# Kernel optimization log

Hardware: AMD Instinct MI355X
Metric: run time of the kernel (lower is better)

Reference implementation:

```python
import jax, jax.numpy as jnp
import numpy as np

DIM_U = 36
IDX_E = np.arange(0, 36, 2)   # even nodes (u1)
IDX_O = np.arange(1, 36, 2)   # odd nodes (u2)
# wraparound neighbor index sets (precomputed mod 36, matching torch negative indexing)
IDX_A = np.arange(-1, 34, 2) % 36   # [35,1,3,...,33]
IDX_B = np.arange(1, 36, 2)         # [1,3,...,35]
IDX_C = np.arange(3, 38, 2) % 36    # [3,5,...,35,1]


def setup_inputs() -> dict:
    key = jax.random.key(0)
    ks = jax.random.split(key, 9)
    N, H = 500000, 128
    return {
        "t": 0,
        "u": jax.random.normal(ks[0], (N, DIM_U), dtype=jnp.float32),
        "reg1": jax.random.normal(ks[1], (6,), dtype=jnp.float32),
        "reg2": jax.random.normal(ks[2], (4,), dtype=jnp.float32),
        "W1": jax.random.normal(ks[3], (18, H), dtype=jnp.float32) * 0.1,
        "b1": jax.random.normal(ks[4], (H,), dtype=jnp.float32) * 0.1,
        "W2a": jax.random.normal(ks[5], (H, 18 * 3), dtype=jnp.float32) * 0.1,
        "b2a": jax.random.normal(ks[6], (18 * 3,), dtype=jnp.float32) * 0.1,
        "W2b": jax.random.normal(ks[7], (H, 18 * 4), dtype=jnp.float32) * 0.1,
        "b2b": jax.random.normal(ks[8], (18 * 4,), dtype=jnp.float32) * 0.1,
    }


def _forward(u, reg1, reg2, W1, b1, W2a, b2a, W2b, b2b):
    N = u.shape[0]
    ie = IDX_E
    # features for even nodes: [N, 18, 5]
    x1 = jnp.stack([
        u[:, ie],
        u[:, (ie + 1) % DIM_U],
        u[:, (ie - 2) % DIM_U] * u[:, (ie - 1) % DIM_U],
        u[:, (ie - 1) % DIM_U] * u[:, (ie + 2) % DIM_U],
        u[:, ie] * u[:, (ie + 1) % DIM_U],
    ], axis=-1)
    io = IDX_O
    # features for odd nodes: [N, 18, 3]
    x2 = jnp.stack([
        u[:, io],
        u[:, (io - 2) % DIM_U] * u[:, (io - 1) % DIM_U],
        u[:, (io - 1) % DIM_U] * u[:, (io + 1) % DIM_U],
    ], axis=-1)
    outreg = jnp.zeros_like(u)
    outreg = outreg.at[:, IDX_E].set(jnp.einsum('nij,j->ni', x1, reg1[1:]) + reg1[0])
    outreg = outreg.at[:, IDX_O].set(jnp.einsum('nij,j->ni', x2, reg2[1:]) + reg2[0])
    # --- neural (cgnn) part: MLP 18 -> H -> (18*3, 18*4) ---
    u1 = u[:, IDX_E]                      # [N, 18]
    h = jnp.tanh(u1 @ W1 + b1)            # [N, H]
    out0 = (h @ W2a + b2a).reshape(N, 18, 3)
    out1 = (h @ W2b + b2b).reshape(N, 18, 4)
    uA, uB, uC = u[:, IDX_A], u[:, IDX_B], u[:, IDX_C]
    outnet = jnp.zeros_like(u)
    outnet = outnet.at[:, IDX_E].set(out0[:, :, 0] + out0[:, :, 1] * uA + out0[:, :, 2] * uB)
    outnet = outnet.at[:, IDX_O].set(out1[:, :, 0] + out1[:, :, 1] * uA + out1[:, :, 2] * uB + out1[:, :, 3] * uC)
    return outnet + outreg


def reference(t, u, reg1, reg2, W1, b1, W2a, b2a, W2b, b2b):
    return _forward(u, reg1, reg2, W1, b1, W2a, b2a, W2b, b2b)
```

## Files before the change

kernel.cpp:

```cpp
#include <hip/hip_runtime.h>
#include <cstddef>


typedef __attribute__((ext_vector_type(8))) __bf16 bf16x8;
typedef __attribute__((ext_vector_type(8))) short short8;
typedef __attribute__((ext_vector_type(4))) float f32x4;

__device__ __forceinline__ unsigned short f2bf(float f) {
    unsigned int u = __float_as_uint(f);
    unsigned int r = (u + 0x7FFFu + ((u >> 16) & 1u)) >> 16;
    return (unsigned short)r;
}

template <typename A>
__device__ __forceinline__ auto mfma_try(A a, A b, f32x4 c, int)
    -> decltype(__builtin_amdgcn_mfma_f32_16x16x32_bf16(a, b, c, 0, 0, 0)) {
    return __builtin_amdgcn_mfma_f32_16x16x32_bf16(a, b, c, 0, 0, 0);
}
template <typename A>
__device__ __forceinline__ f32x4 mfma_try(A a, A b, f32x4 c, long) {
    return __builtin_amdgcn_mfma_f32_16x16x32_bf16(
        __builtin_bit_cast(short8, a), __builtin_bit_cast(short8, b), c, 0, 0, 0);
}
__device__ __forceinline__ f32x4 mfma_bf16(short8 a, short8 b, f32x4 c) {
    return mfma_try(__builtin_bit_cast(bf16x8, a), __builtin_bit_cast(bf16x8, b), c, 0);
}

__device__ __forceinline__ float tanh_fast(float x) {
    const float e2 = __expf(2.0f * x);
    return 1.0f - __fdividef(2.0f, e2 + 1.0f);
}

__global__ __launch_bounds__(256, 4) void mixmodel_mfma6(
    const float* __restrict__ u,
    const float* __restrict__ reg1,
    const float* __restrict__ reg2,
    const float* __restrict__ W1,
    const float* __restrict__ b1,
    const float* __restrict__ W2a,
    const float* __restrict__ b2a,
    const float* __restrict__ W2b,
    const float* __restrict__ b2b,
    float* __restrict__ out,
    int N, int ntiles)
{
    __shared__ __align__(16) float          u_sh[2][32 * 38];
    __shared__ __align__(16) unsigned short h_sh[32 * 136];
    __shared__ __align__(16) float          c2s[32 * 132];

    const int tid = threadIdx.x;
    const int wid = tid >> 6;
    const int l   = tid & 63;
    const int ln  = l & 15;
    const int lg  = l >> 4;
    const int nb  = wid * 32;

    short8 b1f[2];
    short8 b2f[2][4];
    float bias1[2], bias2[2];
#pragma unroll
    for (int t = 0; t < 2; ++t) {
        const int n = nb + t * 16 + ln;
        short8 v;
#pragma unroll
        for (int j = 0; j < 8; ++j) {
            const int k = lg * 8 + j;
            const float w = (k < 18) ? W1[k * 128 + n] : 0.0f;
            v[j] = (short)f2bf(w);
        }
        b1f[t] = v;
        bias1[t] = b1[n];
        bias2[t] = (n < 54) ? b2a[n] : (n < 126 ? b2b[n - 54] : 0.0f);
#pragma unroll
        for (int kk = 0; kk < 4; ++kk) {
            short8 w2;
#pragma unroll
            for (int j = 0; j < 8; ++j) {
                const int k = kk * 32 + lg * 8 + j;
                float w;
                if (n < 54)       w = W2a[k * 54 + n];
                else if (n < 126) w = W2b[k * 72 + (n - 54)];
                else              w = 0.0f;
                w2[j] = (short)f2bf(w);
            }
            b2f[t][kk] = w2;
        }
    }

    const float r10 = reg1[0], r11 = reg1[1], r12 = reg1[2];
    const float r13 = reg1[3], r14 = reg1[4], r15 = reg1[5];
    const float r20 = reg2[0], r21 = reg2[1], r22 = reg2[2], r23 = reg2[3];

    const float4* ug = reinterpret_cast<const float4*>(u);
    const long fmax4 = (long)N * 9 - 1;
    const int gs = gridDim.x;

    const int idx0 = tid;
    const int row0 = idx0 / 9, c0 = idx0 - row0 * 9;
    const int idx1 = 256 + tid;
    const int row1 = idx1 / 9, c1 = idx1 - row1 * 9;

    float4 pf0, pf1;
    {
        long g0 = (long)blockIdx.x * 288 + idx0; if (g0 > fmax4) g0 = fmax4;
        pf0 = ug[g0];
        if (tid < 32) {
            long g1 = (long)blockIdx.x * 288 + idx1; if (g1 > fmax4) g1 = fmax4;
            pf1 = ug[g1];
        }
    }

    int b = 0;
    for (int tile = blockIdx.x; tile < ntiles; tile += gs) {
        {
            float* dst = &u_sh[b][row0 * 38 + c0 * 4];
            reinterpret_cast<float2*>(dst)[0] = make_float2(pf0.x, pf0.y);
            reinterpret_cast<float2*>(dst)[1] = make_float2(pf0.z, pf0.w);
            if (tid < 32) {
                float* dst1 = &u_sh[b][row1 * 38 + c1 * 4];
                reinterpret_cast<float2*>(dst1)[0] = make_float2(pf1.x, pf1.y);
                reinterpret_cast<float2*>(dst1)[1] = make_float2(pf1.z, pf1.w);
            }
            if (tile + gs < ntiles) {
                long g0 = (long)(tile + gs) * 288 + idx0; if (g0 > fmax4) g0 = fmax4;
                pf0 = ug[g0];
                if (tid < 32) {
                    long g1 = (long)(tile + gs) * 288 + idx1; if (g1 > fmax4) g1 = fmax4;
                    pf1 = ug[g1];
                }
            }
        }
        __syncthreads();

#pragma unroll
        for (int rb = 0; rb < 2; ++rb) {
            const float* urow = &u_sh[b][(rb * 16 + ln) * 38];
            short8 a1;
#pragma unroll
            for (int j = 0; j < 8; ++j) {
                const int k = lg * 8 + j;
                const float v = (k < 18) ? urow[2 * k] : 0.0f;
                a1[j] = (short)f2bf(v);
            }
#pragma unroll
            for (int t = 0; t < 2; ++t) {
                f32x4 c = bias1[t];
                const f32x4 h4 = mfma_bf16(a1, b1f[t], c);
#pragma unroll
                for (int r = 0; r < 4; ++r)
                    h_sh[(rb * 16 + lg * 4 + r) * 136 + nb + t * 16 + ln] =
                        f2bf(tanh_fast(h4[r]));
            }
        }
        __syncthreads();

        f32x4 acc2[2][2];
#pragma unroll
        for (int rb = 0; rb < 2; ++rb)
#pragma unroll
            for (int t = 0; t < 2; ++t) acc2[rb][t] = (f32x4)bias2[t];

#pragma unroll
        for (int rb = 0; rb < 2; ++rb) {
            const int arow = rb * 16 + ln;
#pragma unroll
            for (int kk = 0; kk < 4; ++kk) {
                const short8 a2 = *reinterpret_cast<const short8*>(
                    &h_sh[arow * 136 + kk * 32 + lg * 8]);
#pragma unroll
                for (int t = 0; t < 2; ++t)
                    acc2[rb][t] = mfma_bf16(a2, b2f[t][kk], acc2[rb][t]);
            }
        }

#pragma unroll
        for (int rb = 0; rb < 2; ++rb)
#pragma unroll
            for (int t = 0; t < 2; ++t)
#pragma unroll
                for (int r = 0; r < 4; ++r)
                    c2s[(rb * 16 + lg * 4 + r) * 132 + nb + t * 16 + ln] =
                        acc2[rb][t][r];
        __syncthreads();

        const int r0 = tile * 32;
#pragma unroll
        for (int s = 0; s < 3; ++s) {
            const int w = s * 256 + tid;
            if (w < 576) {
                const int row = w / 18;
                const int i   = w - row * 18;
                const int rg  = r0 + row;

                int iA  = 2 * i - 1; if (iA  < 0)   iA  += 36;
                int iM2 = 2 * i - 2; if (iM2 < 0)   iM2 += 36;
                int iP2 = 2 * i + 2; if (iP2 >= 36) iP2 -= 36;
                int iC  = 2 * i + 3; if (iC  >= 36) iC  -= 36;

                const float* uu = &u_sh[b][row * 38];
                const float ue  = uu[2 * i];
                const float uo  = uu[2 * i + 1];
                const float uA  = uu[iA];
                const float um2 = uu[iM2];
                const float up2 = uu[iP2];
                const float uC  = uu[iC];

                const float* c2r = &c2s[row * 132];
                const float o00 = c2r[3 * i], o01 = c2r[3 * i + 1], o02 = c2r[3 * i + 2];
                const float o10 = c2r[54 + 4 * i],     o11 = c2r[54 + 4 * i + 1];
                const float o12 = c2r[54 + 4 * i + 2], o13 = c2r[54 + 4 * i + 3];

                const float oe = o00 + o01 * uA + o02 * uo;
                const float oo = o10 + o11 * uA + o12 * uo + o13 * uC;

                float re = r10;
                re = fmaf(r11, ue,       re);
                re = fmaf(r12, uo,       re);
                re = fmaf(r13, um2 * uA, re);
                re = fmaf(r14, uA * up2, re);
                re = fmaf(r15, ue * uo,  re);

                float ro = r20;
                ro = fmaf(r21, uo,       ro);
                ro = fmaf(r22, uA * ue,  ro);
                ro = fmaf(r23, ue * up2, ro);

                if (rg < N)
                    *reinterpret_cast<float2*>(out + (size_t)rg * 36 + 2 * i) =
                        make_float2(oe + re, oo + ro);
            }
        }
        b ^= 1;
    }
}

extern "C" void kernel_launch(void* const* d_in, const int* in_sizes, int n_in,
                              void* d_out, int out_size, void* d_ws, size_t ws_size,
                              hipStream_t stream) {
    const float* u    = (const float*)d_in[1];
    const float* reg1 = (const float*)d_in[2];
    const float* reg2 = (const float*)d_in[3];
    const float* W1   = (const float*)d_in[4];
    const float* b1   = (const float*)d_in[5];
    const float* W2a  = (const float*)d_in[6];
    const float* b2a  = (const float*)d_in[7];
    const float* W2b  = (const float*)d_in[8];
    const float* b2b  = (const float*)d_in[9];
    float* out = (float*)d_out;

    const int N = in_sizes[1] / 36;
    const int ntiles = (N + 31) / 32;
    int grid = ntiles < 1024 ? ntiles : 1024;
    if (grid < 1) grid = 1;
    mixmodel_mfma6<<<grid, 256, 0, stream>>>(u, reg1, reg2, W1, b1,
                                             W2a, b2a, W2b, b2b, out, N, ntiles);
}
```

Baseline: 85.57 us.

## Use halo-padded u tile, pre-converted bf16 MLP input, and interleaved c2s layout

Stores each u row with wraparound halo columns so the epilogue reads neighbours with vector float2 loads instead of modulo index arithmetic. It also writes a bf16 copy of the even columns at tile load, so the first MFMA operand comes from a single short8 load instead of eight scalar conversions. The second-layer output is scattered into an interleaved per-node layout, so the epilogue reads it with two float4 loads. Double buffering of the u tile is dropped in favour of an extra barrier at the end of each tile, which serialises tile loads against the previous epilogue and adds halo global loads.

```diff
diff --git a/kernel.cpp b/kernel.cpp
--- a/kernel.cpp
+++ b/kernel.cpp
@@ -31,7 +31,7 @@
     return 1.0f - __fdividef(2.0f, e2 + 1.0f);
 }
 
-__global__ __launch_bounds__(256, 4) void mixmodel_mfma6(
+__global__ __launch_bounds__(256, 4) void mixmodel_mfma8(
     const float* __restrict__ u,
     const float* __restrict__ reg1,
     const float* __restrict__ reg2,
@@ -44,9 +44,10 @@
     float* __restrict__ out,
     int N, int ntiles)
 {
-    __shared__ __align__(16) float          u_sh[2][32 * 38];
+    __shared__ __align__(16) float          u_ext[32 * 40];
     __shared__ __align__(16) unsigned short h_sh[32 * 136];
-    __shared__ __align__(16) float          c2s[32 * 132];
+    __shared__ __align__(16) unsigned short u_bf[32 * 32];
+    __shared__ __align__(16) float          c2s[32 * 144];
 
     const int tid = threadIdx.x;
     const int wid = tid >> 6;
@@ -55,9 +56,14 @@
     const int lg  = l >> 4;
     const int nb  = wid * 32;
 
+    reinterpret_cast<unsigned int*>(u_bf)[tid]       = 0u;
+    reinterpret_cast<unsigned int*>(u_bf)[tid + 256] = 0u;
+    __syncthreads();
+
     short8 b1f[2];
     short8 b2f[2][4];
     float bias1[2], bias2[2];
+    int c2idx[2];
 #pragma unroll
     for (int t = 0; t < 2; ++t) {
         const int n = nb + t * 16 + ln;
@@ -71,6 +77,9 @@
         b1f[t] = v;
         bias1[t] = b1[n];
         bias2[t] = (n < 54) ? b2a[n] : (n < 126 ? b2b[n - 54] : 0.0f);
+        if (n < 54)       c2idx[t] = (n / 3) * 8 + (n % 3);
+        else if (n < 126) { const int m = n - 54; c2idx[t] = (m >> 2) * 8 + 4 + (m & 3); }
+        else              c2idx[t] = 3;
 #pragma unroll
         for (int kk = 0; kk < 4; ++kk) {
             short8 w2;
@@ -95,53 +104,62 @@
     const long fmax4 = (long)N * 9 - 1;
     const int gs = gridDim.x;
 
-    const int idx0 = tid;
-    const int row0 = idx0 / 9, c0 = idx0 - row0 * 9;
-    const int idx1 = 256 + tid;
-    const int row1 = idx1 / 9, c1 = idx1 - row1 * 9;
-
-    float4 pf0, pf1;
+    const int row0 = tid / 9,          c0 = tid - row0 * 9;
+    const int row1 = (256 + tid) / 9,  c1 = (256 + tid) - row1 * 9;
+    const int hrow = (tid - 192) >> 1, hside = tid & 1;
+
+    float4 pf0, pf1; float2 pfh;
     {
-        long g0 = (long)blockIdx.x * 288 + idx0; if (g0 > fmax4) g0 = fmax4;
+        const int r0 = blockIdx.x * 32;
+        long g0 = (long)r0 * 9 + tid; if (g0 > fmax4) g0 = fmax4;
         pf0 = ug[g0];
         if (tid < 32) {
-            long g1 = (long)blockIdx.x * 288 + idx1; if (g1 > fmax4) g1 = fmax4;
+            long g1 = (long)r0 * 9 + 256 + tid; if (g1 > fmax4) g1 = fmax4;
             pf1 = ug[g1];
         }
+        if (tid >= 192) {
+            int rr = r0 + hrow; if (rr > N - 1) rr = N - 1;
+            pfh = *reinterpret_cast<const float2*>(u + (size_t)rr * 36 + (hside ? 0 : 34));
+        }
     }
 
-    int b = 0;
     for (int tile = blockIdx.x; tile < ntiles; tile += gs) {
         {
-            float* dst = &u_sh[b][row0 * 38 + c0 * 4];
+            float* dst = &u_ext[row0 * 40 + 2 + c0 * 4];
             reinterpret_cast<float2*>(dst)[0] = make_float2(pf0.x, pf0.y);
             reinterpret_cast<float2*>(dst)[1] = make_float2(pf0.z, pf0.w);
+            reinterpret_cast<unsigned int*>(u_bf)[row0 * 16 + c0] =
+                (unsigned int)f2bf(pf0.x) | ((unsigned int)f2bf(pf0.z) << 16);
             if (tid < 32) {
-                float* dst1 = &u_sh[b][row1 * 38 + c1 * 4];
+                float* dst1 = &u_ext[row1 * 40 + 2 + c1 * 4];
                 reinterpret_cast<float2*>(dst1)[0] = make_float2(pf1.x, pf1.y);
                 reinterpret_cast<float2*>(dst1)[1] = make_float2(pf1.z, pf1.w);
-            }
+                reinterpret_cast<unsigned int*>(u_bf)[row1 * 16 + c1] =
+                    (unsigned int)f2bf(pf1.x) | ((unsigned int)f2bf(pf1.z) << 16);
+            }
+            if (tid >= 192)
+                *reinterpret_cast<float2*>(&u_ext[hrow * 40 + (hside ? 38 : 0)]) = pfh;
+
             if (tile + gs < ntiles) {
-                long g0 = (long)(tile + gs) * 288 + idx0; if (g0 > fmax4) g0 = fmax4;
+                const int r0n = (tile + gs) * 32;
+                long g0 = (long)r0n * 9 + tid; if (g0 > fmax4) g0 = fmax4;
                 pf0 = ug[g0];
                 if (tid < 32) {
-                    long g1 = (long)(tile + gs) * 288 + idx1; if (g1 > fmax4) g1 = fmax4;
+                    long g1 = (long)r0n * 9 + 256 + tid; if (g1 > fmax4) g1 = fmax4;
                     pf1 = ug[g1];
                 }
+                if (tid >= 192) {
+                    int rr = r0n + hrow; if (rr > N - 1) rr = N - 1;
+                    pfh = *reinterpret_cast<const float2*>(u + (size_t)rr * 36 + (hside ? 0 : 34));
+                }
             }
         }
         __syncthreads();
 
 #pragma unroll
         for (int rb = 0; rb < 2; ++rb) {
-            const float* urow = &u_sh[b][(rb * 16 + ln) * 38];
-            short8 a1;
-#pragma unroll
-            for (int j = 0; j < 8; ++j) {
-                const int k = lg * 8 + j;
-                const float v = (k < 18) ? urow[2 * k] : 0.0f;
-                a1[j] = (short)f2bf(v);
-            }
+            const short8 a1 = *reinterpret_cast<const short8*>(
+                &u_bf[(rb * 16 + ln) * 32 + lg * 8]);
 #pragma unroll
             for (int t = 0; t < 2; ++t) {
                 f32x4 c = bias1[t];
@@ -179,8 +197,7 @@
             for (int t = 0; t < 2; ++t)
 #pragma unroll
                 for (int r = 0; r < 4; ++r)
-                    c2s[(rb * 16 + lg * 4 + r) * 132 + nb + t * 16 + ln] =
-                        acc2[rb][t][r];
+                    c2s[(rb * 16 + lg * 4 + r) * 144 + c2idx[t]] = acc2[rb][t][r];
         __syncthreads();
 
         const int r0 = tile * 32;
@@ -192,26 +209,18 @@
                 const int i   = w - row * 18;
                 const int rg  = r0 + row;
 
-                int iA  = 2 * i - 1; if (iA  < 0)   iA  += 36;
-                int iM2 = 2 * i - 2; if (iM2 < 0)   iM2 += 36;
-                int iP2 = 2 * i + 2; if (iP2 >= 36) iP2 -= 36;
-                int iC  = 2 * i + 3; if (iC  >= 36) iC  -= 36;
-
-                const float* uu = &u_sh[b][row * 38];
-                const float ue  = uu[2 * i];
-                const float uo  = uu[2 * i + 1];
-                const float uA  = uu[iA];
-                const float um2 = uu[iM2];
-                const float up2 = uu[iP2];
-                const float uC  = uu[iC];
-
-                const float* c2r = &c2s[row * 132];
-                const float o00 = c2r[3 * i], o01 = c2r[3 * i + 1], o02 = c2r[3 * i + 2];
-                const float o10 = c2r[54 + 4 * i],     o11 = c2r[54 + 4 * i + 1];
-                const float o12 = c2r[54 + 4 * i + 2], o13 = c2r[54 + 4 * i + 3];
-
-                const float oe = o00 + o01 * uA + o02 * uo;
-                const float oo = o10 + o11 * uA + o12 * uo + o13 * uC;
+                const float2 v0 = *reinterpret_cast<const float2*>(&u_ext[row * 40 + 2 * i]);
+                const float2 v1 = *reinterpret_cast<const float2*>(&u_ext[row * 40 + 2 * i + 2]);
+                const float2 v2 = *reinterpret_cast<const float2*>(&u_ext[row * 40 + 2 * i + 4]);
+                const f32x4  q0 = *reinterpret_cast<const f32x4*>(&c2s[row * 144 + 8 * i]);
+                const f32x4  q1 = *reinterpret_cast<const f32x4*>(&c2s[row * 144 + 8 * i + 4]);
+
+                const float um2 = v0.x, uA = v0.y;
+                const float ue  = v1.x, uo = v1.y;
+                const float up2 = v2.x, uC = v2.y;
+
+                const float oe = q0[0] + q0[1] * uA + q0[2] * uo;
+                const float oo = q1[0] + q1[1] * uA + q1[2] * uo + q1[3] * uC;
 
                 float re = r10;
                 re = fmaf(r11, ue,       re);
@@ -230,7 +239,7 @@
                         make_float2(oe + re, oo + ro);
             }
         }
-        b ^= 1;
+        __syncthreads();
     }
 }
 
@@ -252,6 +261,6 @@
     const int ntiles = (N + 31) / 32;
     int grid = ntiles < 1024 ? ntiles : 1024;
     if (grid < 1) grid = 1;
-    mixmodel_mfma6<<<grid, 256, 0, stream>>>(u, reg1, reg2, W1, b1,
+    mixmodel_mfma8<<<grid, 256, 0, stream>>>(u, reg1, reg2, W1, b1,
                                              W2a, b2a, W2b, b2b, out, N, ntiles);
 }
```

Measured after the change: 80.73 us. 1.06x faster.
